# Kernel optimization log

Measured on AMD Instinct MI355X. Metric: run time of the kernel, lower is better.

## Reference

```python
import math
import jax, jax.numpy as jnp
import numpy as np

B, S, D, H = 2, 2048, 1024, 16
HD = D // H


def setup_inputs() -> dict:
    key = jax.random.key(0)
    ks = jax.random.split(key, 12)
    w = lambda k: jax.random.normal(k, (D, D), jnp.float32) * 0.02
    return {
        "query": jax.random.normal(ks[0], (B, S, D), jnp.float32),
        "key": jax.random.normal(ks[1], (B, S, D), jnp.float32),
        "value": jax.random.normal(ks[2], (B, S, D), jnp.float32),
        "mask": jax.random.randint(ks[3], (B, 1, S, S), 0, 2, jnp.int32),
        "relative_pos_bias": jax.random.normal(ks[4], (S, S, H), jnp.float32) * 0.1,
        "Wq": w(ks[5]), "bq": jnp.zeros((D,), jnp.float32),
        "Wk": w(ks[6]), "bk": jnp.zeros((D,), jnp.float32),
        "Wv": w(ks[7]), "bv": jnp.zeros((D,), jnp.float32),
        "Wo": w(ks[8]), "bo": jnp.zeros((D,), jnp.float32),
    }


def reference(query, key, value, mask, relative_pos_bias,
              Wq, bq, Wk, bk, Wv, bv, Wo, bo):
    b, s, d = query.shape
    h = relative_pos_bias.shape[-1]
    hd = d // h
    scale = math.sqrt(hd)
    # projections -> (b, h, s, hd)
    split = lambda x: x.reshape(b, s, h, hd).transpose(0, 2, 1, 3)
    Q = split(query @ Wq + bq)
    K = split(key @ Wk + bk)
    V = split(value @ Wv + bv)
    scores = jnp.einsum("bhqd,bhkd->bhqk", Q, K) / scale
    # torch: bias.unsqueeze(0).transpose(1,3) => scores[b,h,i,j] += bias[j,i,h]
    scores = scores + jnp.transpose(relative_pos_bias, (2, 1, 0))[None]
    scores = jnp.where(mask == 0, jnp.float32(-1e9), scores)
    attn = jax.nn.softmax(scores, axis=-1)
    out = jnp.einsum("bhqk,bhkd->bhqd", attn, V)
    out = out.transpose(0, 2, 1, 3).reshape(b, s, d)
    return out @ Wo + bo
```

## Files before the change

### kernel.cpp

```cpp
#include <hip/hip_runtime.h>
#include <math.h>

#define SS 2048
#define DD 1024
#define HH 16

typedef _Float16 f16;
typedef _Float16 half8 __attribute__((ext_vector_type(8)));
typedef _Float16 half4 __attribute__((ext_vector_type(4)));
typedef float f32x4 __attribute__((ext_vector_type(4)));
typedef unsigned long long u64;

#define LOG2E 1.44269504f
#define MASKNEG -30000.0f

__device__ __forceinline__ void gload16(const void* g, void* lds) {
    __builtin_amdgcn_global_load_lds(
        (const __attribute__((address_space(1))) unsigned int*)g,
        (__attribute__((address_space(3))) unsigned int*)lds, 16, 0, 0);
}

__global__ __launch_bounds__(256)
void cvt_x(const float* __restrict__ q, const float* __restrict__ k,
           const float* __restrict__ v, f16* __restrict__ oq,
           f16* __restrict__ ok, f16* __restrict__ ov)
{
    const int z = blockIdx.z;
    const float* src = z == 0 ? q : z == 1 ? k : v;
    f16* dst = z == 0 ? oq : z == 1 ? ok : ov;
    size_t i = ((size_t)blockIdx.x * 256 + threadIdx.x) * 8;
    float4 v0 = *reinterpret_cast<const float4*>(src + i);
    float4 v1 = *reinterpret_cast<const float4*>(src + i + 4);
    half8 h;
    h[0] = (f16)v0.x; h[1] = (f16)v0.y; h[2] = (f16)v0.z; h[3] = (f16)v0.w;
    h[4] = (f16)v1.x; h[5] = (f16)v1.y; h[6] = (f16)v1.z; h[7] = (f16)v1.w;
    *reinterpret_cast<half8*>(dst + i) = h;
}

__global__ __launch_bounds__(256)
void cvt_wT(const float* __restrict__ wq, const float* __restrict__ wk,
            const float* __restrict__ wv, const float* __restrict__ wo,
            f16* __restrict__ oq, f16* __restrict__ ok,
            f16* __restrict__ ov, f16* __restrict__ oo)
{
    __shared__ float Lt[64][65];
    const int z = blockIdx.z;
    const float* W = z == 0 ? wq : z == 1 ? wk : z == 2 ? wv : wo;
    f16* WT = z == 0 ? oq : z == 1 ? ok : z == 2 ? ov : oo;
    const int n0 = blockIdx.x * 64, k0 = blockIdx.y * 64;
    const int t = threadIdx.x;
    {
        int row = t >> 2;
        int c0  = (t & 3) * 16;
#pragma unroll
        for (int u = 0; u < 4; ++u) {
            float4 x = *reinterpret_cast<const float4*>(
                &W[(size_t)(k0 + row) * DD + n0 + c0 + u * 4]);
            Lt[row][c0 + u * 4 + 0] = x.x;
            Lt[row][c0 + u * 4 + 1] = x.y;
            Lt[row][c0 + u * 4 + 2] = x.z;
            Lt[row][c0 + u * 4 + 3] = x.w;
        }
    }
    __syncthreads();
    {
        int n  = t >> 2;
        int kc = (t & 3) * 16;
        half8 h0, h1;
#pragma unroll
        for (int u = 0; u < 8; ++u) h0[u] = (f16)Lt[kc + u][n];
#pragma unroll
        for (int u = 0; u < 8; ++u) h1[u] = (f16)Lt[kc + 8 + u][n];
        f16* dst = &WT[(size_t)(n0 + n) * DD + k0 + kc];
        *reinterpret_cast<half8*>(dst) = h0;
        *reinterpret_cast<half8*>(dst + 8) = h1;
    }
}

__global__ __launch_bounds__(256)
void cvt_rpbT3(const float* __restrict__ rpb, f16* __restrict__ rpbT)
{
    __shared__ f16 Lt[16][16][66];
    const int t = threadIdx.x, wid = t >> 6, l = t & 63;
    const int i0 = blockIdx.x * 16;
    const int j0 = blockIdx.y * 64;
    const int il = l >> 2;
    const int h0 = (l & 3) * 4;
#pragma unroll
    for (int p = 0; p < 16; ++p) {
        int jl = p * 4 + wid;
        float4 v = *reinterpret_cast<const float4*>(
            rpb + ((size_t)(j0 + jl) * SS + i0 + il) * HH + h0);
        Lt[h0 + 0][il][jl] = (f16)(v.x * LOG2E);
        Lt[h0 + 1][il][jl] = (f16)(v.y * LOG2E);
        Lt[h0 + 2][il][jl] = (f16)(v.z * LOG2E);
        Lt[h0 + 3][il][jl] = (f16)(v.w * LOG2E);
    }
    __syncthreads();
    const int part = t & 7;
#pragma unroll
    for (int p = 0; p < 8; ++p) {
        int rowid = p * 32 + (t >> 3);
        int h = rowid >> 4, i2 = rowid & 15;
        half8 v;
#pragma unroll
        for (int e = 0; e < 8; ++e) {
            int sig = 32 * (part & 1) + 16 * (e >> 2) + 4 * (part >> 1) + (e & 3);
            v[e] = Lt[h][i2][sig];
        }
        *reinterpret_cast<half8*>(
            rpbT + ((size_t)h * SS + i0 + i2) * SS + j0 + part * 8) = v;
    }
}

__global__ __launch_bounds__(256)
void cvt_maskbits(const int* __restrict__ mask, u64* __restrict__ mb)
{
    const int t = threadIdx.x, wid = t >> 6, l = t & 63;
    const int row = blockIdx.x * 4 + wid;
    const int* src = mask + (size_t)row * SS;
    u64* dst = mb + (size_t)row * 32;
    for (int it = 0; it < 32; ++it) {
        int mv = src[it * 64 + l];
        u64 bal = __ballot(mv != 0);
        if (l == 0) dst[it] = bal;
    }
}

__global__ __launch_bounds__(256)
void proj3(const f16* __restrict__ Xq, const f16* __restrict__ Xk,
           const f16* __restrict__ Xv, const f16* __restrict__ WqT,
           const f16* __restrict__ WkT, const f16* __restrict__ WvT,
           const float* __restrict__ bq, const float* __restrict__ bk,
           const float* __restrict__ bv,
           f16* __restrict__ Qo, f16* __restrict__ Ko, f16* __restrict__ VTo)
{
    __shared__ f16 As[128 * 64];
    __shared__ f16 Bs[128 * 64];
    const int t = threadIdx.x, wid = t >> 6, l = t & 63, c = l & 15, g = l >> 4;
    const int gz = blockIdx.z;
    const f16 *Ap, *Bp; const float* bias; int m0, n0;
    if (gz == 2) { Ap = WvT; Bp = Xv; bias = bv; m0 = blockIdx.x * 128; n0 = blockIdx.y * 128; }
    else if (gz == 1) { Ap = Xk; Bp = WkT; bias = bk; m0 = blockIdx.y * 128; n0 = blockIdx.x * 128; }
    else { Ap = Xq; Bp = WqT; bias = bq; m0 = blockIdx.y * 128; n0 = blockIdx.x * 128; }
    const int wm = wid >> 1, wn = wid & 1;
    f32x4 acc[4][4] = {};
    char* AsB = (char*)As; char* BsB = (char*)Bs;

    for (int k0 = 0; k0 < DD; k0 += 64) {
        __syncthreads();
#pragma unroll
        for (int j = 0; j < 4; ++j) {
            int row = wid * 32 + j * 8 + (l >> 3);
            int slot = (l & 7) ^ (row & 7);
            gload16(Ap + (size_t)(m0 + row) * DD + k0 + slot * 8,
                    AsB + (wid * 32 + j * 8) * 128);
            gload16(Bp + (size_t)(n0 + row) * DD + k0 + slot * 8,
                    BsB + (wid * 32 + j * 8) * 128);
        }
        __syncthreads();
#pragma unroll
        for (int ks = 0; ks < 2; ++ks) {
            half8 af[4];
#pragma unroll
            for (int mt = 0; mt < 4; ++mt) {
                int row = wm * 64 + mt * 16 + c;
                af[mt] = *(const half8*)(AsB + row * 128 +
                         ((ks * 64 + g * 16) ^ ((row & 7) << 4)));
            }
#pragma unroll
            for (int nt = 0; nt < 4; ++nt) {
                int row = wn * 64 + nt * 16 + c;
                half8 bf = *(const half8*)(BsB + row * 128 +
                           ((ks * 64 + g * 16) ^ ((row & 7) << 4)));
#pragma unroll
                for (int mt = 0; mt < 4; ++mt)
                    acc[mt][nt] = __builtin_amdgcn_mfma_f32_16x16x32_f16(
                        af[mt], bf, acc[mt][nt], 0, 0, 0);
            }
        }
    }

    const float post = (gz == 0) ? 0.125f * LOG2E : 1.0f;
    if (gz < 2) {
        f16* dst = gz ? Ko : Qo;
#pragma unroll
        for (int nt = 0; nt < 4; ++nt) {
            int n = n0 + wn * 64 + nt * 16 + c;
            float bn = bias[n];
            int h = n >> 6, hd = n & 63;
#pragma unroll
            for (int mt = 0; mt < 4; ++mt)
#pragma unroll
                for (int reg = 0; reg < 4; ++reg) {
                    int m = m0 + wm * 64 + mt * 16 + 4 * g + reg;
                    int b = m >> 11, s = m & (SS - 1);
                    dst[(((size_t)(b * HH + h)) * SS + s) * 64 + hd] =
                        (f16)((acc[mt][nt][reg] + bn) * post);
                }
        }
    } else {
#pragma unroll
        for (int mt = 0; mt < 4; ++mt)
#pragma unroll
            for (int reg = 0; reg < 4; ++reg) {
                int m = m0 + wm * 64 + mt * 16 + 4 * g + reg;
                float bd = bias[m];
                int h = m >> 6, dl = m & 63;
#pragma unroll
                for (int nt = 0; nt < 4; ++nt) {
                    int n = n0 + wn * 64 + nt * 16 + c;
                    int b = n >> 11, s = n & (SS - 1);
                    VTo[(((size_t)(b * HH + h)) * 64 + dl) * SS + s] =
                        (f16)(acc[mt][nt][reg] + bd);
                }
            }
    }
}

__global__ __launch_bounds__(256, 4)
void attn_fwd(const f16* __restrict__ Qw, const f16* __restrict__ Kw,
              const f16* __restrict__ VTw, const f16* __restrict__ rpbT,
              const u64* __restrict__ mbits, f16* __restrict__ AOh)
{
    __shared__ f16 Ks[2][64 * 64];
    __shared__ f16 Vs[2][64 * 64];

    const int t = threadIdx.x, wid = t >> 6, l = t & 63, c = l & 15, g = l >> 4;
    const int bh = blockIdx.x, b = bh >> 4, h = bh & 15;
    const int q0 = blockIdx.y * 64;
    const size_t baseSD = (size_t)bh * SS * 64;
    const size_t baseDS = (size_t)bh * 64 * SS;
    const f16* Kbase = Kw + baseSD;
    const f16* Vbase = VTw + baseDS;

    const int qrow_c = q0 + wid * 16 + c;
    const f16* bp = rpbT + (size_t)h * SS * SS + (size_t)qrow_c * SS + g * 16;
    const u64* mp = mbits + ((size_t)b * SS + qrow_c) * 32;

    const int s     = l & 7;
    const int srow0 = wid * 16 + (l >> 3);
    const int sswz  = (srow0 & 7) << 4;
    const int kdst  = (s << 4) ^ sswz;
    const int velo  = 32 * (s >> 2) + 16 * (s & 1) + 4 * ((s >> 1) & 1);
    const int vdlo  = (velo * 2) ^ sswz;
    const int vdhi  = (velo * 2 + 16) ^ sswz;

    int ga[4];
#pragma unroll
    for (int r = 0; r < 4; ++r) ga[r] = (g * 4 + r) * 4;

    half8 qf[2];
    qf[0] = *(const half8*)(Qw + baseSD + (size_t)qrow_c * 64 + g * 8);
    qf[1] = *(const half8*)(Qw + baseSD + (size_t)qrow_c * 64 + 32 + g * 8);

    {
        half8 k0 = *(const half8*)(Kbase + (size_t)srow0 * 64 + s * 8);
        half8 k1 = *(const half8*)(Kbase + (size_t)(srow0 + 8) * 64 + s * 8);
        half8 v0 = *(const half8*)(Vbase + (size_t)srow0 * SS + s * 8);
        half8 v1 = *(const half8*)(Vbase + (size_t)(srow0 + 8) * SS + s * 8);
        char* kd = (char*)Ks[0]; char* vd = (char*)Vs[0];
        *(half8*)(kd + srow0 * 128 + kdst) = k0;
        *(half8*)(kd + (srow0 + 8) * 128 + kdst) = k1;
        half4 lo0 = {v0[0], v0[1], v0[2], v0[3]}, hi0 = {v0[4], v0[5], v0[6], v0[7]};
        half4 lo1 = {v1[0], v1[1], v1[2], v1[3]}, hi1 = {v1[4], v1[5], v1[6], v1[7]};
        *(half4*)(vd + srow0 * 128 + vdlo) = lo0;
        *(half4*)(vd + srow0 * 128 + vdhi) = hi0;
        *(half4*)(vd + (srow0 + 8) * 128 + vdlo) = lo1;
        *(half4*)(vd + (srow0 + 8) * 128 + vdhi) = hi1;
    }
    half8 bb0 = *(const half8*)(bp);
    half8 bb1 = *(const half8*)(bp + 8);
    u64 mm = mp[0];
    __syncthreads();

    f32x4 acc[4] = {};
    float mrow = -INFINITY, lp = 0.f;
    const int shg = 4 * g;

    int buf = 0;
    for (int kt = 0; kt < SS / 64; ++kt) {
        const bool more = (kt + 1 < SS / 64);
        const int jn = more ? (kt + 1) * 64 : 0;
        const int ktn = more ? kt + 1 : 0;

        half8 k0n = *(const half8*)(Kbase + (size_t)(jn + srow0) * 64 + s * 8);
        half8 k1n = *(const half8*)(Kbase + (size_t)(jn + srow0 + 8) * 64 + s * 8);
        half8 v0n = *(const half8*)(Vbase + (size_t)srow0 * SS + jn + s * 8);
        half8 v1n = *(const half8*)(Vbase + (size_t)(srow0 + 8) * SS + jn + s * 8);
        half8 bbn0 = *(const half8*)(bp + jn);
        half8 bbn1 = *(const half8*)(bp + jn + 8);
        u64 mmn = mp[ktn];

        char* KsB = (char*)Ks[buf];
        char* VsB = (char*)Vs[buf];

        u64 sh = mm >> shg;
        f32x4 sc[4];
#pragma unroll
        for (int nt = 0; nt < 4; ++nt)
#pragma unroll
            for (int r = 0; r < 4; ++r) {
                float bf = (float)(nt < 2 ? bb0[nt * 4 + r] : bb1[(nt - 2) * 4 + r]);
                sc[nt][r] = ((sh >> (16 * nt + r)) & 1) ? bf : MASKNEG;
            }

        __builtin_amdgcn_s_setprio(1);
#pragma unroll
        for (int ks = 0; ks < 2; ++ks)
#pragma unroll
            for (int nt = 0; nt < 4; ++nt) {
                int row = nt * 16 + c;
                half8 kf = *(const half8*)(KsB + row * 128 +
                           ((ks * 64 + g * 16) ^ ((row & 7) << 4)));
                sc[nt] = __builtin_amdgcn_mfma_f32_16x16x32_f16(
                    kf, qf[ks], sc[nt], 0, 0, 0);
            }
        __builtin_amdgcn_s_setprio(0);

        float rm = fmaxf(fmaxf(fmaxf(sc[0][0], sc[0][1]), fmaxf(sc[0][2], sc[0][3])),
                         fmaxf(fmaxf(sc[1][0], sc[1][1]), fmaxf(sc[1][2], sc[1][3])));
        rm = fmaxf(rm, fmaxf(fmaxf(fmaxf(sc[2][0], sc[2][1]), fmaxf(sc[2][2], sc[2][3])),
                             fmaxf(fmaxf(sc[3][0], sc[3][1]), fmaxf(sc[3][2], sc[3][3]))));
        rm = fmaxf(rm, __shfl_xor(rm, 16));
        rm = fmaxf(rm, __shfl_xor(rm, 32));
        if (!__all(rm <= mrow + 8.0f)) {
            float mn = fmaxf(mrow, rm);
            float scal = exp2f(mrow - mn);
            mrow = mn;
            lp *= scal;
            float sq[4];
#pragma unroll
            for (int r = 0; r < 4; ++r)
                sq[r] = __int_as_float(__builtin_amdgcn_ds_bpermute(
                            ga[r], __float_as_int(scal)));
#pragma unroll
            for (int nt = 0; nt < 4; ++nt)
#pragma unroll
                for (int r = 0; r < 4; ++r) acc[nt][r] *= sq[r];
        }
        float psum = 0.f;
#pragma unroll
        for (int nt = 0; nt < 4; ++nt)
#pragma unroll
            for (int r = 0; r < 4; ++r) {
                float p = exp2f(sc[nt][r] - mrow);
                sc[nt][r] = p;
                psum += p;
            }
        lp += psum;

        half4 pa[4];
#pragma unroll
        for (int kk = 0; kk < 4; ++kk) {
            half4 pv = {(f16)sc[kk][0], (f16)sc[kk][1],
                        (f16)sc[kk][2], (f16)sc[kk][3]};
            pa[kk] = pv;
        }

        __builtin_amdgcn_s_setprio(1);
#pragma unroll
        for (int ks = 0; ks < 2; ++ks)
#pragma unroll
            for (int nt2 = 0; nt2 < 4; ++nt2) {
                int row = nt2 * 16 + c;
                half8 vf = *(const half8*)(VsB + row * 128 +
                           ((ks * 64 + g * 16) ^ ((row & 7) << 4)));
                half4 vlo = {vf[0], vf[1], vf[2], vf[3]};
                half4 vhi = {vf[4], vf[5], vf[6], vf[7]};
                acc[nt2] = __builtin_amdgcn_mfma_f32_16x16x16f16(
                    pa[2 * ks], vlo, acc[nt2], 0, 0, 0);
                acc[nt2] = __builtin_amdgcn_mfma_f32_16x16x16f16(
                    pa[2 * ks + 1], vhi, acc[nt2], 0, 0, 0);
            }
        __builtin_amdgcn_s_setprio(0);

        if (more) {
            char* kd = (char*)Ks[buf ^ 1];
            char* vd = (char*)Vs[buf ^ 1];
            *(half8*)(kd + srow0 * 128 + kdst) = k0n;
            *(half8*)(kd + (srow0 + 8) * 128 + kdst) = k1n;
            half4 lo0 = {v0n[0], v0n[1], v0n[2], v0n[3]}, hi0 = {v0n[4], v0n[5], v0n[6], v0n[7]};
            half4 lo1 = {v1n[0], v1n[1], v1n[2], v1n[3]}, hi1 = {v1n[4], v1n[5], v1n[6], v1n[7]};
            *(half4*)(vd + srow0 * 128 + vdlo) = lo0;
            *(half4*)(vd + srow0 * 128 + vdhi) = hi0;
            *(half4*)(vd + (srow0 + 8) * 128 + vdlo) = lo1;
            *(half4*)(vd + (srow0 + 8) * 128 + vdhi) = hi1;
            buf ^= 1;
            bb0 = bbn0; bb1 = bbn1; mm = mmn;
        }
        __syncthreads();
    }

    float lt = lp;
    lt += __shfl_xor(lt, 16);
    lt += __shfl_xor(lt, 32);
    float linv[4];
#pragma unroll
    for (int r = 0; r < 4; ++r)
        linv[r] = 1.0f / __int_as_float(__builtin_amdgcn_ds_bpermute(
                      ga[r], __float_as_int(lt)));
#pragma unroll
    for (int r = 0; r < 4; ++r) {
        int qrow = q0 + wid * 16 + 4 * g + r;
#pragma unroll
        for (int nt2 = 0; nt2 < 4; ++nt2)
            AOh[((size_t)b * SS + qrow) * DD + h * 64 + nt2 * 16 + c] =
                (f16)(acc[nt2][r] * linv[r]);
    }
}

__global__ __launch_bounds__(256)
void gemm_out(const f16* __restrict__ A, const f16* __restrict__ BT,
              const float* __restrict__ bias, float* __restrict__ out)
{
    __shared__ f16 As[128 * 64];
    __shared__ f16 Bs[128 * 64];
    const int t = threadIdx.x, wid = t >> 6, l = t & 63, c = l & 15, g = l >> 4;
    const int m0 = blockIdx.y * 128, n0 = blockIdx.x * 128;
    const int wm = wid >> 1, wn = wid & 1;
    f32x4 acc[4][4] = {};
    char* AsB = (char*)As; char* BsB = (char*)Bs;

    for (int k0 = 0; k0 < DD; k0 += 64) {
        __syncthreads();
#pragma unroll
        for (int j = 0; j < 4; ++j) {
            int row = wid * 32 + j * 8 + (l >> 3);
            int slot = (l & 7) ^ (row & 7);
            gload16(A + (size_t)(m0 + row) * DD + k0 + slot * 8,
                    AsB + (wid * 32 + j * 8) * 128);
            gload16(BT + (size_t)(n0 + row) * DD + k0 + slot * 8,
                    BsB + (wid * 32 + j * 8) * 128);
        }
        __syncthreads();
#pragma unroll
        for (int ks = 0; ks < 2; ++ks) {
            half8 af[4];
#pragma unroll
            for (int mt = 0; mt < 4; ++mt) {
                int row = wm * 64 + mt * 16 + c;
                af[mt] = *(const half8*)(AsB + row * 128 +
                         ((ks * 64 + g * 16) ^ ((row & 7) << 4)));
            }
#pragma unroll
            for (int nt = 0; nt < 4; ++nt) {
                int row = wn * 64 + nt * 16 + c;
                half8 bf = *(const half8*)(BsB + row * 128 +
                           ((ks * 64 + g * 16) ^ ((row & 7) << 4)));
#pragma unroll
                for (int mt = 0; mt < 4; ++mt)
                    acc[mt][nt] = __builtin_amdgcn_mfma_f32_16x16x32_f16(
                        af[mt], bf, acc[mt][nt], 0, 0, 0);
            }
        }
    }
#pragma unroll
    for (int nt = 0; nt < 4; ++nt) {
        int n = n0 + wn * 64 + nt * 16 + c;
        float bn = bias[n];
#pragma unroll
        for (int mt = 0; mt < 4; ++mt)
#pragma unroll
            for (int reg = 0; reg < 4; ++reg) {
                int m = m0 + wm * 64 + mt * 16 + 4 * g + reg;
                out[(size_t)m * DD + n] = acc[mt][nt][reg] + bn;
            }
    }
}

extern "C" void kernel_launch(void* const* d_in, const int* in_sizes, int n_in,
                              void* d_out, int out_size, void* d_ws, size_t ws_size,
                              hipStream_t stream)
{
    (void)in_sizes; (void)n_in; (void)out_size; (void)ws_size;

    const float* query = (const float*)d_in[0];
    const float* key   = (const float*)d_in[1];
    const float* value = (const float*)d_in[2];
    const int*   mask  = (const int*)d_in[3];
    const float* rpb   = (const float*)d_in[4];
    const float* Wq = (const float*)d_in[5];  const float* bq = (const float*)d_in[6];
    const float* Wk = (const float*)d_in[7];  const float* bk = (const float*)d_in[8];
    const float* Wv = (const float*)d_in[9];  const float* bv = (const float*)d_in[10];
    const float* Wo = (const float*)d_in[11]; const float* bo = (const float*)d_in[12];
    float* out = (float*)d_out;

    const size_t NX = (size_t)2 * SS * DD;
    const size_t NW = (size_t)DD * DD;
    f16* Xq    = (f16*)d_ws;
    f16* Xk    = Xq + NX;
    f16* Xv    = Xk + NX;
    f16* WqT   = Xv + NX;
    f16* WkT   = WqT + NW;
    f16* WvT   = WkT + NW;
    f16* WoT   = WvT + NW;
    f16* Qw    = WoT + NW;
    f16* Kw    = Qw + NX;
    f16* VTw   = Kw + NX;
    f16* rpbT  = VTw + NX;
    u64* mbits = (u64*)(rpbT + (size_t)HH * SS * SS);
    f16* AOh   = Xq;

    cvt_x<<<dim3(NX / 2048, 1, 3), 256, 0, stream>>>(query, key, value, Xq, Xk, Xv);
    cvt_wT<<<dim3(16, 16, 4), 256, 0, stream>>>(Wq, Wk, Wv, Wo, WqT, WkT, WvT, WoT);
    cvt_rpbT3<<<dim3(SS / 16, SS / 64), 256, 0, stream>>>(rpb, rpbT);
    cvt_maskbits<<<dim3((2 * SS) / 4), 256, 0, stream>>>(mask, mbits);
    proj3<<<dim3(8, 32, 3), 256, 0, stream>>>(Xq, Xk, Xv, WqT, WkT, WvT,
                                              bq, bk, bv, Qw, Kw, VTw);
    attn_fwd<<<dim3(2 * HH, SS / 64), 256, 0, stream>>>(Qw, Kw, VTw, rpbT, mbits, AOh);
    gemm_out<<<dim3(8, 32), 256, 0, stream>>>(AOh, WoT, bo, out);
}
```

Baseline: 297.6 us.

## Process two 64-row query tiles per attention block to reuse K/V tiles

Each attention workgroup now handles 128 query rows, as two interleaved 64-row sets with separate softmax state and accumulators. Every K/V tile staged in LDS feeds twice as many MFMAs, halving K/V global traffic and LDS staging per query row. The grid is reordered so consecutive blocks share a head, and launch bounds drop to 2 waves per SIMD to fit the doubled register footprint. The costs are fewer workgroups (512), lower occupancy, and more register pressure with possible spills.

```diff
diff --git a/kernel.cpp b/kernel.cpp
--- a/kernel.cpp
+++ b/kernel.cpp
@@ -218,7 +218,7 @@
     }
 }
 
-__global__ __launch_bounds__(256, 4)
+__global__ __launch_bounds__(256, 2)
 void attn_fwd(const f16* __restrict__ Qw, const f16* __restrict__ Kw,
               const f16* __restrict__ VTw, const f16* __restrict__ rpbT,
               const u64* __restrict__ mbits, f16* __restrict__ AOh)
@@ -227,16 +227,19 @@
     __shared__ f16 Vs[2][64 * 64];
 
     const int t = threadIdx.x, wid = t >> 6, l = t & 63, c = l & 15, g = l >> 4;
-    const int bh = blockIdx.x, b = bh >> 4, h = bh & 15;
-    const int q0 = blockIdx.y * 64;
+    const int bh = blockIdx.y, b = bh >> 4, h = bh & 15;
+    const int q0 = blockIdx.x * 128;
     const size_t baseSD = (size_t)bh * SS * 64;
     const size_t baseDS = (size_t)bh * 64 * SS;
     const f16* Kbase = Kw + baseSD;
     const f16* Vbase = VTw + baseDS;
 
-    const int qrow_c = q0 + wid * 16 + c;
-    const f16* bp = rpbT + (size_t)h * SS * SS + (size_t)qrow_c * SS + g * 16;
-    const u64* mp = mbits + ((size_t)b * SS + qrow_c) * 32;
+    const int qrowA = q0 + wid * 16 + c;
+    const int qrowB = qrowA + 64;
+    const f16* bpA = rpbT + (size_t)h * SS * SS + (size_t)qrowA * SS + g * 16;
+    const f16* bpB = bpA + (size_t)64 * SS;
+    const u64* mpA = mbits + ((size_t)b * SS + qrowA) * 32;
+    const u64* mpB = mpA + 64 * 32;
 
     const int s     = l & 7;
     const int srow0 = wid * 16 + (l >> 3);
@@ -250,9 +253,11 @@
 #pragma unroll
     for (int r = 0; r < 4; ++r) ga[r] = (g * 4 + r) * 4;
 
-    half8 qf[2];
-    qf[0] = *(const half8*)(Qw + baseSD + (size_t)qrow_c * 64 + g * 8);
-    qf[1] = *(const half8*)(Qw + baseSD + (size_t)qrow_c * 64 + 32 + g * 8);
+    half8 qfA[2], qfB[2];
+    qfA[0] = *(const half8*)(Qw + baseSD + (size_t)qrowA * 64 + g * 8);
+    qfA[1] = *(const half8*)(Qw + baseSD + (size_t)qrowA * 64 + 32 + g * 8);
+    qfB[0] = *(const half8*)(Qw + baseSD + (size_t)qrowB * 64 + g * 8);
+    qfB[1] = *(const half8*)(Qw + baseSD + (size_t)qrowB * 64 + 32 + g * 8);
 
     {
         half8 k0 = *(const half8*)(Kbase + (size_t)srow0 * 64 + s * 8);
@@ -269,13 +274,16 @@
         *(half4*)(vd + (srow0 + 8) * 128 + vdlo) = lo1;
         *(half4*)(vd + (srow0 + 8) * 128 + vdhi) = hi1;
     }
-    half8 bb0 = *(const half8*)(bp);
-    half8 bb1 = *(const half8*)(bp + 8);
-    u64 mm = mp[0];
+    half8 bbA0 = *(const half8*)(bpA);
+    half8 bbA1 = *(const half8*)(bpA + 8);
+    half8 bbB0 = *(const half8*)(bpB);
+    half8 bbB1 = *(const half8*)(bpB + 8);
+    u64 mmA = mpA[0], mmB = mpB[0];
     __syncthreads();
 
-    f32x4 acc[4] = {};
-    float mrow = -INFINITY, lp = 0.f;
+    f32x4 accA[4] = {}, accB[4] = {};
+    float mrowA = -INFINITY, lpA = 0.f;
+    float mrowB = -INFINITY, lpB = 0.f;
     const int shg = 4 * g;
 
     int buf = 0;
@@ -288,21 +296,25 @@
         half8 k1n = *(const half8*)(Kbase + (size_t)(jn + srow0 + 8) * 64 + s * 8);
         half8 v0n = *(const half8*)(Vbase + (size_t)srow0 * SS + jn + s * 8);
         half8 v1n = *(const half8*)(Vbase + (size_t)(srow0 + 8) * SS + jn + s * 8);
-        half8 bbn0 = *(const half8*)(bp + jn);
-        half8 bbn1 = *(const half8*)(bp + jn + 8);
-        u64 mmn = mp[ktn];
+        half8 bbnA0 = *(const half8*)(bpA + jn);
+        half8 bbnA1 = *(const half8*)(bpA + jn + 8);
+        half8 bbnB0 = *(const half8*)(bpB + jn);
+        half8 bbnB1 = *(const half8*)(bpB + jn + 8);
+        u64 mmnA = mpA[ktn], mmnB = mpB[ktn];
 
         char* KsB = (char*)Ks[buf];
         char* VsB = (char*)Vs[buf];
 
-        u64 sh = mm >> shg;
-        f32x4 sc[4];
+        u64 shA = mmA >> shg, shB = mmB >> shg;
+        f32x4 scA[4], scB[4];
 #pragma unroll
         for (int nt = 0; nt < 4; ++nt)
 #pragma unroll
             for (int r = 0; r < 4; ++r) {
-                float bf = (float)(nt < 2 ? bb0[nt * 4 + r] : bb1[(nt - 2) * 4 + r]);
-                sc[nt][r] = ((sh >> (16 * nt + r)) & 1) ? bf : MASKNEG;
+                float bfA = (float)(nt < 2 ? bbA0[nt * 4 + r] : bbA1[(nt - 2) * 4 + r]);
+                float bfB = (float)(nt < 2 ? bbB0[nt * 4 + r] : bbB1[(nt - 2) * 4 + r]);
+                scA[nt][r] = ((shA >> (16 * nt + r)) & 1) ? bfA : MASKNEG;
+                scB[nt][r] = ((shB >> (16 * nt + r)) & 1) ? bfB : MASKNEG;
             }
 
         __builtin_amdgcn_s_setprio(1);
@@ -313,49 +325,91 @@
                 int row = nt * 16 + c;
                 half8 kf = *(const half8*)(KsB + row * 128 +
                            ((ks * 64 + g * 16) ^ ((row & 7) << 4)));
-                sc[nt] = __builtin_amdgcn_mfma_f32_16x16x32_f16(
-                    kf, qf[ks], sc[nt], 0, 0, 0);
+                scA[nt] = __builtin_amdgcn_mfma_f32_16x16x32_f16(
+                    kf, qfA[ks], scA[nt], 0, 0, 0);
+                scB[nt] = __builtin_amdgcn_mfma_f32_16x16x32_f16(
+                    kf, qfB[ks], scB[nt], 0, 0, 0);
             }
         __builtin_amdgcn_s_setprio(0);
 
-        float rm = fmaxf(fmaxf(fmaxf(sc[0][0], sc[0][1]), fmaxf(sc[0][2], sc[0][3])),
-                         fmaxf(fmaxf(sc[1][0], sc[1][1]), fmaxf(sc[1][2], sc[1][3])));
-        rm = fmaxf(rm, fmaxf(fmaxf(fmaxf(sc[2][0], sc[2][1]), fmaxf(sc[2][2], sc[2][3])),
-                             fmaxf(fmaxf(sc[3][0], sc[3][1]), fmaxf(sc[3][2], sc[3][3]))));
-        rm = fmaxf(rm, __shfl_xor(rm, 16));
-        rm = fmaxf(rm, __shfl_xor(rm, 32));
-        if (!__all(rm <= mrow + 8.0f)) {
-            float mn = fmaxf(mrow, rm);
-            float scal = exp2f(mrow - mn);
-            mrow = mn;
-            lp *= scal;
-            float sq[4];
-#pragma unroll
-            for (int r = 0; r < 4; ++r)
-                sq[r] = __int_as_float(__builtin_amdgcn_ds_bpermute(
-                            ga[r], __float_as_int(scal)));
+        half4 paA[4], paB[4];
+        {
+            float rm = fmaxf(fmaxf(fmaxf(scA[0][0], scA[0][1]), fmaxf(scA[0][2], scA[0][3])),
+                             fmaxf(fmaxf(scA[1][0], scA[1][1]), fmaxf(scA[1][2], scA[1][3])));
+            rm = fmaxf(rm, fmaxf(fmaxf(fmaxf(scA[2][0], scA[2][1]), fmaxf(scA[2][2], scA[2][3])),
+                                 fmaxf(fmaxf(scA[3][0], scA[3][1]), fmaxf(scA[3][2], scA[3][3]))));
+            rm = fmaxf(rm, __shfl_xor(rm, 16));
+            rm = fmaxf(rm, __shfl_xor(rm, 32));
+            if (!__all(rm <= mrowA + 8.0f)) {
+                float mn = fmaxf(mrowA, rm);
+                float scal = exp2f(mrowA - mn);
+                mrowA = mn;
+                lpA *= scal;
+                float sq[4];
+#pragma unroll
+                for (int r = 0; r < 4; ++r)
+                    sq[r] = __int_as_float(__builtin_amdgcn_ds_bpermute(
+                                ga[r], __float_as_int(scal)));
+#pragma unroll
+                for (int nt = 0; nt < 4; ++nt)
+#pragma unroll
+                    for (int r = 0; r < 4; ++r) accA[nt][r] *= sq[r];
+            }
+            float psum = 0.f;
 #pragma unroll
             for (int nt = 0; nt < 4; ++nt)
 #pragma unroll
-                for (int r = 0; r < 4; ++r) acc[nt][r] *= sq[r];
-        }
-        float psum = 0.f;
-#pragma unroll
-        for (int nt = 0; nt < 4; ++nt)
-#pragma unroll
-            for (int r = 0; r < 4; ++r) {
-                float p = exp2f(sc[nt][r] - mrow);
-                sc[nt][r] = p;
-                psum += p;
-            }
-        lp += psum;
-
-        half4 pa[4];
-#pragma unroll
-        for (int kk = 0; kk < 4; ++kk) {
-            half4 pv = {(f16)sc[kk][0], (f16)sc[kk][1],
-                        (f16)sc[kk][2], (f16)sc[kk][3]};
-            pa[kk] = pv;
+                for (int r = 0; r < 4; ++r) {
+                    float p = exp2f(scA[nt][r] - mrowA);
+                    scA[nt][r] = p;
+                    psum += p;
+                }
+            lpA += psum;
+#pragma unroll
+            for (int kk = 0; kk < 4; ++kk) {
+                half4 pv = {(f16)scA[kk][0], (f16)scA[kk][1],
+                            (f16)scA[kk][2], (f16)scA[kk][3]};
+                paA[kk] = pv;
+            }
+        }
+        {
+            float rm = fmaxf(fmaxf(fmaxf(scB[0][0], scB[0][1]), fmaxf(scB[0][2], scB[0][3])),
+                             fmaxf(fmaxf(scB[1][0], scB[1][1]), fmaxf(scB[1][2], scB[1][3])));
+            rm = fmaxf(rm, fmaxf(fmaxf(fmaxf(scB[2][0], scB[2][1]), fmaxf(scB[2][2], scB[2][3])),
+                                 fmaxf(fmaxf(scB[3][0], scB[3][1]), fmaxf(scB[3][2], scB[3][3]))));
+            rm = fmaxf(rm, __shfl_xor(rm, 16));
+            rm = fmaxf(rm, __shfl_xor(rm, 32));
+            if (!__all(rm <= mrowB + 8.0f)) {
+                float mn = fmaxf(mrowB, rm);
+                float scal = exp2f(mrowB - mn);
+                mrowB = mn;
+                lpB *= scal;
+                float sq[4];
+#pragma unroll
+                for (int r = 0; r < 4; ++r)
+                    sq[r] = __int_as_float(__builtin_amdgcn_ds_bpermute(
+                                ga[r], __float_as_int(scal)));
+#pragma unroll
+                for (int nt = 0; nt < 4; ++nt)
+#pragma unroll
+                    for (int r = 0; r < 4; ++r) accB[nt][r] *= sq[r];
+            }
+            float psum = 0.f;
+#pragma unroll
+            for (int nt = 0; nt < 4; ++nt)
+#pragma unroll
+                for (int r = 0; r < 4; ++r) {
+                    float p = exp2f(scB[nt][r] - mrowB);
+                    scB[nt][r] = p;
+                    psum += p;
+                }
+            lpB += psum;
+#pragma unroll
+            for (int kk = 0; kk < 4; ++kk) {
+                half4 pv = {(f16)scB[kk][0], (f16)scB[kk][1],
+                            (f16)scB[kk][2], (f16)scB[kk][3]};
+                paB[kk] = pv;
+            }
         }
 
         __builtin_amdgcn_s_setprio(1);
@@ -368,10 +422,14 @@
                            ((ks * 64 + g * 16) ^ ((row & 7) << 4)));
                 half4 vlo = {vf[0], vf[1], vf[2], vf[3]};
                 half4 vhi = {vf[4], vf[5], vf[6], vf[7]};
-                acc[nt2] = __builtin_amdgcn_mfma_f32_16x16x16f16(
-                    pa[2 * ks], vlo, acc[nt2], 0, 0, 0);
-                acc[nt2] = __builtin_amdgcn_mfma_f32_16x16x16f16(
-                    pa[2 * ks + 1], vhi, acc[nt2], 0, 0, 0);
+                accA[nt2] = __builtin_amdgcn_mfma_f32_16x16x16f16(
+                    paA[2 * ks], vlo, accA[nt2], 0, 0, 0);
+                accA[nt2] = __builtin_amdgcn_mfma_f32_16x16x16f16(
+                    paA[2 * ks + 1], vhi, accA[nt2], 0, 0, 0);
+                accB[nt2] = __builtin_amdgcn_mfma_f32_16x16x16f16(
+                    paB[2 * ks], vlo, accB[nt2], 0, 0, 0);
+                accB[nt2] = __builtin_amdgcn_mfma_f32_16x16x16f16(
+                    paB[2 * ks + 1], vhi, accB[nt2], 0, 0, 0);
             }
         __builtin_amdgcn_s_setprio(0);
 
@@ -387,26 +445,47 @@
             *(half4*)(vd + (srow0 + 8) * 128 + vdlo) = lo1;
             *(half4*)(vd + (srow0 + 8) * 128 + vdhi) = hi1;
             buf ^= 1;
-            bb0 = bbn0; bb1 = bbn1; mm = mmn;
+            bbA0 = bbnA0; bbA1 = bbnA1; bbB0 = bbnB0; bbB1 = bbnB1;
+            mmA = mmnA; mmB = mmnB;
         }
         __syncthreads();
     }
 
-    float lt = lp;
-    lt += __shfl_xor(lt, 16);
-    lt += __shfl_xor(lt, 32);
-    float linv[4];
-#pragma unroll
-    for (int r = 0; r < 4; ++r)
-        linv[r] = 1.0f / __int_as_float(__builtin_amdgcn_ds_bpermute(
-                      ga[r], __float_as_int(lt)));
-#pragma unroll
-    for (int r = 0; r < 4; ++r) {
-        int qrow = q0 + wid * 16 + 4 * g + r;
-#pragma unroll
-        for (int nt2 = 0; nt2 < 4; ++nt2)
-            AOh[((size_t)b * SS + qrow) * DD + h * 64 + nt2 * 16 + c] =
-                (f16)(acc[nt2][r] * linv[r]);
+    {
+        float lt = lpA;
+        lt += __shfl_xor(lt, 16);
+        lt += __shfl_xor(lt, 32);
+        float linv[4];
+#pragma unroll
+        for (int r = 0; r < 4; ++r)
+            linv[r] = 1.0f / __int_as_float(__builtin_amdgcn_ds_bpermute(
+                          ga[r], __float_as_int(lt)));
+#pragma unroll
+        for (int r = 0; r < 4; ++r) {
+            int qrow = q0 + wid * 16 + 4 * g + r;
+#pragma unroll
+            for (int nt2 = 0; nt2 < 4; ++nt2)
+                AOh[((size_t)b * SS + qrow) * DD + h * 64 + nt2 * 16 + c] =
+                    (f16)(accA[nt2][r] * linv[r]);
+        }
+    }
+    {
+        float lt = lpB;
+        lt += __shfl_xor(lt, 16);
+        lt += __shfl_xor(lt, 32);
+        float linv[4];
+#pragma unroll
+        for (int r = 0; r < 4; ++r)
+            linv[r] = 1.0f / __int_as_float(__builtin_amdgcn_ds_bpermute(
+                          ga[r], __float_as_int(lt)));
+#pragma unroll
+        for (int r = 0; r < 4; ++r) {
+            int qrow = q0 + 64 + wid * 16 + 4 * g + r;
+#pragma unroll
+            for (int nt2 = 0; nt2 < 4; ++nt2)
+                AOh[((size_t)b * SS + qrow) * DD + h * 64 + nt2 * 16 + c] =
+                    (f16)(accB[nt2][r] * linv[r]);
+        }
     }
 }
 
@@ -508,6 +587,6 @@
     cvt_maskbits<<<dim3((2 * SS) / 4), 256, 0, stream>>>(mask, mbits);
     proj3<<<dim3(8, 32, 3), 256, 0, stream>>>(Xq, Xk, Xv, WqT, WkT, WvT,
                                               bq, bk, bv, Qw, Kw, VTw);
-    attn_fwd<<<dim3(2 * HH, SS / 64), 256, 0, stream>>>(Qw, Kw, VTw, rpbT, mbits, AOh);
+    attn_fwd<<<dim3(SS / 128, 2 * HH), 256, 0, stream>>>(Qw, Kw, VTw, rpbT, mbits, AOh);
     gemm_out<<<dim3(8, 32), 256, 0, stream>>>(AOh, WoT, bo, out);
 }
```

Measured after the change: 302.9 us. About the same (+1.8%).
